# Kernel optimization log

Hardware: AMD Instinct MI355X
Metric: run time of the kernel (lower is better)

The kernel has to match this reference:

```python
import jax, jax.numpy as jnp
import numpy as np

D = 2048          # hidden_size
I = 8192          # expert_intermediate_size
E = 8             # num_experts
TOP_K = 2
N_CONST = 2       # ConstantExpert count (CONSTANT=2); experts: [copy, zero, ce0, ce1, shared_mlp x (E-4)]


def setup_inputs() -> dict:
    key = jax.random.key(0)
    ks = jax.random.split(key, 9)
    s = 0.02
    return {
        "hidden_states": jax.random.normal(ks[0], (2, 2048, D), dtype=jnp.float32),
        "gate_w1": jax.random.normal(ks[1], (D, E * 8), dtype=jnp.float32) * s,
        "gate_w2": jax.random.normal(ks[2], (E * 8, E), dtype=jnp.float32) * s,
        "ce_wg": jax.random.normal(ks[3], (N_CONST, D, 2), dtype=jnp.float32) * s,
        "ce_const": jax.random.normal(ks[4], (N_CONST, D), dtype=jnp.float32),
        "w_gate": jax.random.normal(ks[5], (D, I), dtype=jnp.float32) * s,
        "w_up": jax.random.normal(ks[6], (D, I), dtype=jnp.float32) * s,
        "w_down": jax.random.normal(ks[7], (I, D), dtype=jnp.float32) * s,
    }


def reference(hidden_states, gate_w1, gate_w2, ce_wg, ce_const, w_gate, w_up, w_down):
    B, S, d = hidden_states.shape
    x = hidden_states.reshape(-1, d).astype(jnp.float32)          # [N, D] tokens

    # Router: MLP gate (fp32) -> softmax -> top-2
    router_logits = jnp.tanh(x @ gate_w1) @ gate_w2               # [N, E]
    probs = jax.nn.softmax(router_logits, axis=-1)
    topw, topi = jax.lax.top_k(probs, TOP_K)                      # [N, 2]
    # mask out last expert (idx == E-1), renormalize
    topw = jnp.where(topi == E - 1, jnp.zeros_like(topw), topw)
    topw = topw / jnp.sum(topw, axis=-1, keepdims=True)
    # per-expert combined routing weight (top-k indices are distinct)
    pe = jnp.sum(topw[..., None] * jax.nn.one_hot(topi, E, dtype=topw.dtype), axis=1)  # [N, E]

    def const_expert(wg, c):
        cw = jax.nn.softmax(x @ wg, axis=-1)                      # [N, 2]
        return cw[:, :1] * x + cw[:, 1:] * c[None, :]

    # shared SwiGLU expert (all dense experts share the same weights in the source)
    swiglu = (jax.nn.silu(x @ w_gate) * (x @ w_up)) @ w_down      # [N, D]

    out = (pe[:, 0:1] * x                                          # CopyExpert (expert 1 = ZeroExpert contributes 0)
           + pe[:, 2:3] * const_expert(ce_wg[0], ce_const[0])
           + pe[:, 3:4] * const_expert(ce_wg[1], ce_const[1])
           + jnp.sum(pe[:, 4:], axis=1, keepdims=True) * swiglu)   # shared dense experts 4..E-1
    return out.reshape(B, S, d), router_logits
```

## Files before the change

kernel.cpp:

```cpp
#include <hip/hip_runtime.h>
#include <stdint.h>
#include <stddef.h>

#define TOKS 4096
#define DH   2048
#define DI   8192

typedef __attribute__((ext_vector_type(8))) short short8v;
typedef __attribute__((ext_vector_type(4))) short short4v;
typedef __attribute__((ext_vector_type(4))) float floatx4;

__device__ __forceinline__ float b2f(short s) {
  union { unsigned u; float f; } v;
  v.u = ((unsigned)(unsigned short)s) << 16;
  return v.f;
}
__device__ __forceinline__ short f2b(float f) {
  union { float f; unsigned u; } v; v.f = f;
  unsigned r = (v.u + 0x7fffu + ((v.u >> 16) & 1u)) >> 16;
  return (short)(unsigned short)r;
}
__device__ __forceinline__ void gload_lds16(const void* g, void* l) {
  __builtin_amdgcn_global_load_lds((const __attribute__((address_space(1))) void*)g,
                                   (__attribute__((address_space(3))) void*)l, 16, 0, 0);
}

__global__ __launch_bounds__(256) void cvt_f32_to_bf16(const float* __restrict__ in,
                                                       short* __restrict__ out) {
  size_t i = (size_t)blockIdx.x * 256 + threadIdx.x;
  floatx4 v = *(const floatx4*)&in[i * 4];
  short4v o;
  o[0] = f2b(v[0]); o[1] = f2b(v[1]); o[2] = f2b(v[2]); o[3] = f2b(v[3]);
  *(short4v*)&out[i * 4] = o;
}

__global__ __launch_bounds__(256) void transpose_to_bf16(const float* __restrict__ in,
                                                         short* __restrict__ out,
                                                         int K, int N,
                                                         int rstride, int roff) {
  __shared__ float tile[32][33];
  const int n0 = blockIdx.x * 32, k0 = blockIdx.y * 32;
  const int tx = threadIdx.x & 31, ty = threadIdx.x >> 5;
#pragma unroll
  for (int yy = 0; yy < 32; yy += 8)
    tile[ty + yy][tx] = in[(size_t)(k0 + ty + yy) * N + n0 + tx];
  __syncthreads();
#pragma unroll
  for (int yy = 0; yy < 32; yy += 8)
    out[((size_t)(n0 + ty + yy) * rstride + roff) * K + k0 + tx] = f2b(tile[tx][ty + yy]);
}

#define RT_TPB 8
__global__ __launch_bounds__(256) void router_kernel(const float* __restrict__ x,
                                                     const float* __restrict__ gw1,
                                                     const float* __restrict__ gw2,
                                                     const float* __restrict__ cwg,
                                                     float* __restrict__ logits_out,
                                                     float* __restrict__ coef) {
  const int wave = threadIdx.x >> 6, lane = threadIdx.x & 63;
  const int tok0 = blockIdx.x * RT_TPB;
  __shared__ float xs[RT_TPB][512];
  __shared__ float ll[RT_TPB][8];
  __shared__ float cd[RT_TPB][4];

  float tj[2] = {0.f, 0.f};
  float cda[2][4] = {{0.f,0.f,0.f,0.f},{0.f,0.f,0.f,0.f}};

  const int st = threadIdx.x >> 5;
  const int sl = threadIdx.x & 31;

  for (int c = 0; c < 4; ++c) {
    const int dbase = c * 512;
#pragma unroll
    for (int r = 0; r < 4; ++r) {
      const int idx = r * 128 + sl * 4;
      *(floatx4*)&xs[st][idx] = *(const floatx4*)&x[(size_t)(tok0 + st) * DH + dbase + idx];
    }
    __syncthreads();
    for (int d = 0; d < 512; ++d) {
      const float g = gw1[(size_t)(dbase + d) * 64 + lane];
      tj[0] += xs[wave * 2 + 0][d] * g;
      tj[1] += xs[wave * 2 + 1][d] * g;
    }
#pragma unroll
    for (int dq = 0; dq < 8; ++dq) {
      const int d = dq * 64 + lane;
      const float w0 = cwg[(size_t)(dbase + d) * 2 + 0];
      const float w1 = cwg[(size_t)(dbase + d) * 2 + 1];
      const float w2 = cwg[(size_t)DH * 2 + (dbase + d) * 2 + 0];
      const float w3 = cwg[(size_t)DH * 2 + (dbase + d) * 2 + 1];
#pragma unroll
      for (int t = 0; t < 2; ++t) {
        const float xv = xs[wave * 2 + t][d];
        cda[t][0] += xv * w0; cda[t][1] += xv * w1;
        cda[t][2] += xv * w2; cda[t][3] += xv * w3;
      }
    }
    __syncthreads();
  }

#pragma unroll
  for (int t = 0; t < 2; ++t) {
    const float th = tanhf(tj[t]);
#pragma unroll
    for (int e = 0; e < 8; ++e) {
      float p = th * gw2[lane * 8 + e];
      for (int off = 32; off; off >>= 1) p += __shfl_xor(p, off);
      if (lane == 0) ll[wave * 2 + t][e] = p;
    }
#pragma unroll
    for (int dd = 0; dd < 4; ++dd) {
      float p = cda[t][dd];
      for (int off = 32; off; off >>= 1) p += __shfl_xor(p, off);
      if (lane == 0) cd[wave * 2 + t][dd] = p;
    }
  }
  __syncthreads();

  if (threadIdx.x < RT_TPB) {
    const int t = threadIdx.x;
    const int gtok = tok0 + t;
    float l[8];
#pragma unroll
    for (int e = 0; e < 8; ++e) l[e] = ll[t][e];
#pragma unroll
    for (int e = 0; e < 8; ++e) logits_out[(size_t)gtok * 8 + e] = l[e];
    float m = l[0];
#pragma unroll
    for (int e = 1; e < 8; ++e) m = fmaxf(m, l[e]);
    float p[8], s = 0.f;
#pragma unroll
    for (int e = 0; e < 8; ++e) { p[e] = expf(l[e] - m); s += p[e]; }
#pragma unroll
    for (int e = 0; e < 8; ++e) p[e] /= s;
    int i1 = 0;
#pragma unroll
    for (int e = 1; e < 8; ++e) if (p[e] > p[i1]) i1 = e;
    int i2 = -1;
#pragma unroll
    for (int e = 0; e < 8; ++e) {
      if (e == i1) continue;
      if (i2 < 0 || p[e] > p[i2]) i2 = e;
    }
    float w1 = (i1 == 7) ? 0.f : p[i1];
    float w2 = (i2 == 7) ? 0.f : p[i2];
    const float nrm = w1 + w2;
    w1 /= nrm; w2 /= nrm;
    float pe[8];
#pragma unroll
    for (int e = 0; e < 8; ++e) pe[e] = 0.f;
    pe[i1] += w1; pe[i2] += w2;
    const float cw00 = 1.f / (1.f + expf(cd[t][1] - cd[t][0]));
    const float cw10 = 1.f / (1.f + expf(cd[t][3] - cd[t][2]));
    coef[gtok * 4 + 0] = pe[0] + pe[2] * cw00 + pe[3] * cw10;
    coef[gtok * 4 + 1] = pe[2] * (1.f - cw00);
    coef[gtok * 4 + 2] = pe[3] * (1.f - cw10);
    coef[gtok * 4 + 3] = pe[4] + pe[5] + pe[6] + pe[7];
  }
}

__global__ __launch_bounds__(512, 2) void gemm1_gu_silu(const short* __restrict__ A,
                                                        const short* __restrict__ Bt,
                                                        short* __restrict__ H,
                                                        int K, int lda, int ldb) {
  __shared__ __align__(16) short As[2][256 * 64];
  __shared__ __align__(16) short Bs[2][256 * 64];

  const int wave = threadIdx.x >> 6;
  const int lane = threadIdx.x & 63;
  const int wm64 = (wave >> 2) * 64;
  const int wn32 = (wave & 3) * 32;
  const int l15 = lane & 15;
  const int quad = lane >> 4;
  const int rq = l15 & 7;
  const int qoff0 = (quad ^ rq) * 8;
  const int qoff1 = ((4 + quad) ^ rq) * 8;

  const int srow = lane >> 3;
  const int scol = ((lane & 7) ^ srow) * 8;

  const int cpx = gridDim.x >> 3;
  const int wg = ((int)blockIdx.x & 7) * cpx + ((int)blockIdx.x >> 3);
  const int m0 = (wg & 15) * 256;
  const int n0 = (wg >> 4) * 256;

  const short* pA = A + (size_t)(m0 + wave * 16 + srow) * lda + scol;
  const short* pB = Bt + (size_t)(n0 + wave * 16 + srow) * ldb + scol;

  floatx4 acc[8][4];
#pragma unroll
  for (int i = 0; i < 8; ++i)
#pragma unroll
    for (int j = 0; j < 4; ++j) acc[i][j] = (floatx4)0.f;

  short8v a[4][2];
  short8v b[4][2];

#define STAGE_A(buf, half, k0)                                                  \
  {                                                                             \
    _Pragma("unroll") for (int g = 0; g < 2; ++g)                               \
        gload_lds16(pA + (size_t)((half) * 128 + g * 8) * lda + (k0),           \
                    &As[buf][((half) * 128 + wave * 16 + g * 8) * 64]);         \
  }
#define STAGE_B(buf, half, k0)                                                  \
  {                                                                             \
    _Pragma("unroll") for (int g = 0; g < 2; ++g)                               \
        gload_lds16(pB + (size_t)((half) * 128 + g * 8) * ldb + (k0),           \
                    &Bs[buf][((half) * 128 + wave * 16 + g * 8) * 64]);         \
  }
#define READ_A(buf, half)                                                       \
  {                                                                             \
    _Pragma("unroll") for (int mi = 0; mi < 4; ++mi) {                          \
      const int r = (half) * 128 + wm64 + mi * 16 + l15;                        \
      a[mi][0] = *(const short8v*)&As[buf][r * 64 + qoff0];                     \
      a[mi][1] = *(const short8v*)&As[buf][r * 64 + qoff1];                     \
    }                                                                           \
  }
#define READ_BALL(buf)                                                          \
  {                                                                             \
    _Pragma("unroll") for (int h = 0; h < 2; ++h)                               \
    _Pragma("unroll") for (int ni = 0; ni < 2; ++ni) {                          \
      const int r = h * 128 + wn32 + ni * 16 + l15;                             \
      b[h * 2 + ni][0] = *(const short8v*)&Bs[buf][r * 64 + qoff0];             \
      b[h * 2 + ni][1] = *(const short8v*)&Bs[buf][r * 64 + qoff1];             \
    }                                                                           \
  }
#define MFMA_H(mh)                                                              \
  {                                                                             \
    __builtin_amdgcn_s_setprio(1);                                              \
    _Pragma("unroll") for (int kk = 0; kk < 2; ++kk)                            \
    _Pragma("unroll") for (int mi = 0; mi < 4; ++mi)                            \
    _Pragma("unroll") for (int ni = 0; ni < 4; ++ni)                            \
        acc[(mh) * 4 + mi][ni] = __builtin_amdgcn_mfma_f32_16x16x32_bf16(       \
            a[mi][kk], b[ni][kk], acc[(mh) * 4 + mi][ni], 0, 0, 0);             \
    __builtin_amdgcn_s_setprio(0);                                              \
  }
#define BAR __builtin_amdgcn_s_barrier()
#define LGKM0 asm volatile("s_waitcnt lgkmcnt(0)" ::: "memory")
#define VMC(n) asm volatile("s_waitcnt vmcnt(" #n ")" ::: "memory")

#define KTILE(t, MODE)                                                          \
  {                                                                             \
    const int buf = (t) & 1, nbuf = buf ^ 1;                                    \
    const int k1 = ((t) + 1) * 64, k2 = ((t) + 2) * 64;                         \
    (void)k1; (void)k2; (void)nbuf;                                             \
                                                          \
    READ_A(buf, 0); READ_BALL(buf);                                             \
    if (MODE <= 1) { STAGE_B(nbuf, 1, k1); STAGE_A(nbuf, 1, k1); }              \
    BAR; LGKM0; MFMA_H(0); BAR;                                                 \
                                                          \
    READ_A(buf, 1);                                                             \
    if (MODE == 0) { STAGE_A(buf, 0, k2); STAGE_B(buf, 0, k2); VMC(4); }        \
    if (MODE == 1) { VMC(0); }                                                  \
    BAR; LGKM0; MFMA_H(1); BAR;                                                 \
  }

  STAGE_A(0, 0, 0); STAGE_B(0, 0, 0); STAGE_B(0, 1, 0); STAGE_A(0, 1, 0);
  STAGE_A(1, 0, 64); STAGE_B(1, 0, 64);
  VMC(4);
  BAR;

  const int NT = K >> 6;
  for (int t = 0; t < NT - 2; ++t) KTILE(t, 0);
  KTILE(NT - 2, 1);
  KTILE(NT - 1, 2);

#undef KTILE
#undef STAGE_A
#undef STAGE_B
#undef READ_A
#undef READ_BALL
#undef MFMA_H

  const int q4 = quad * 4;
#pragma unroll
  for (int mi = 0; mi < 8; ++mi) {
    const int row0 = m0 + (mi >> 2) * 128 + wm64 + (mi & 3) * 16 + q4;
#pragma unroll
    for (int ni = 0; ni < 4; ++ni) {
      const int col = n0 + (ni >> 1) * 128 + wn32 + (ni & 1) * 16 + l15;
#pragma unroll
      for (int rg = 0; rg < 4; ++rg) {
        const float v = acc[mi][ni][rg];
        const float p = __shfl_xor(v, 1);
        if ((l15 & 1) == 0) {
          const float hv = (v / (1.f + __expf(-v))) * p;
          H[(size_t)(row0 + rg) * DI + (col >> 1)] = f2b(hv);
        }
      }
    }
  }
}

__device__ __forceinline__ void gemm_mainloop(const short* __restrict__ A,
                                              const short* __restrict__ Bt,
                                              int K, int lda, int ldb,
                                              int m0, int n0,
                                              short* As, short* Bs,
                                              floatx4 (&acc)[4][4]) {
  const int wave = threadIdx.x >> 6;
  const int lane = threadIdx.x & 63;
  const int srow = lane >> 3;
  const int scol = ((lane & 7) ^ srow) * 8;
  const int wm = (wave & 1) * 64;
  const int wn = (wave >> 1) * 64;
  const int l15 = lane & 15;
  const int quad = lane >> 4;
  const int q0 = ((quad ^ (l15 & 7)) * 8);

  for (int k0 = 0; k0 < K; k0 += 64) {
#pragma unroll
    for (int q = 0; q < 4; ++q) {
      const int chunk = wave * 4 + q;
      const int row = chunk * 8 + srow;
      gload_lds16(A + (size_t)(m0 + row) * lda + k0 + scol, &As[chunk * 8 * 64]);
      gload_lds16(Bt + (size_t)(n0 + row) * ldb + k0 + scol, &Bs[chunk * 8 * 64]);
    }
    __syncthreads();
#pragma unroll
    for (int kk = 0; kk < 2; ++kk) {
      const int qo = q0 ^ (kk * 32);
      short8v af[4], bf[4];
#pragma unroll
      for (int i = 0; i < 4; ++i) {
        af[i] = *(const short8v*)&As[(wm + i * 16 + l15) * 64 + qo];
        bf[i] = *(const short8v*)&Bs[(wn + i * 16 + l15) * 64 + qo];
      }
#pragma unroll
      for (int mi = 0; mi < 4; ++mi)
#pragma unroll
        for (int ni = 0; ni < 4; ++ni)
          acc[mi][ni] = __builtin_amdgcn_mfma_f32_16x16x32_bf16(af[mi], bf[ni],
                                                                acc[mi][ni], 0, 0, 0);
    }
    __syncthreads();
  }
}

__global__ __launch_bounds__(256) void gemm_bt_moe(const short* __restrict__ A,
                                                   const short* __restrict__ Bt,
                                                   float* __restrict__ out,
                                                   const float* __restrict__ x,
                                                   const float* __restrict__ cc,
                                                   const float* __restrict__ coef,
                                                   int K, int lda, int ldb) {
  __shared__ short As[128 * 64];
  __shared__ short Bs[128 * 64];
  floatx4 acc[4][4];
#pragma unroll
  for (int a = 0; a < 4; ++a)
#pragma unroll
    for (int b = 0; b < 4; ++b) acc[a][b] = (floatx4)0.0f;
  const int lin = blockIdx.y * gridDim.x + blockIdx.x;
  const int m0 = (lin & 31) * 128, n0 = (lin >> 5) * 128;
  gemm_mainloop(A, Bt, K, lda, ldb, m0, n0, As, Bs, acc);
  const int wave = threadIdx.x >> 6, lane = threadIdx.x & 63;
  const int wm = (wave & 1) * 64, wn = (wave >> 1) * 64;
  const int l15 = lane & 15, q4 = (lane >> 4) * 4;
#pragma unroll
  for (int mi = 0; mi < 4; ++mi) {
    const int row0 = m0 + wm + mi * 16 + q4;
#pragma unroll
    for (int ni = 0; ni < 4; ++ni) {
      const int col = n0 + wn + ni * 16 + l15;
      const float c0v = cc[col];
      const float c1v = cc[DH + col];
#pragma unroll
      for (int rg = 0; rg < 4; ++rg) {
        const int row = row0 + rg;
        const floatx4 cf = *(const floatx4*)&coef[row * 4];
        out[(size_t)row * DH + col] =
            cf[0] * x[(size_t)row * DH + col] + cf[1] * c0v + cf[2] * c1v +
            cf[3] * acc[mi][ni][rg];
      }
    }
  }
}

extern "C" void kernel_launch(void* const* d_in, const int* in_sizes, int n_in,
                              void* d_out, int out_size, void* d_ws, size_t ws_size,
                              hipStream_t stream) {
  const float* x   = (const float*)d_in[0];
  const float* gw1 = (const float*)d_in[1];
  const float* gw2 = (const float*)d_in[2];
  const float* cwg = (const float*)d_in[3];
  const float* cc  = (const float*)d_in[4];
  const float* wg  = (const float*)d_in[5];
  const float* wu  = (const float*)d_in[6];
  const float* wd  = (const float*)d_in[7];
  float* out = (float*)d_out;
  float* logits_out = out + (size_t)TOKS * DH;

  char* ws = (char*)d_ws;
  short* xb    = (short*)(ws);
  short* wgwuT = (short*)(ws + 16777216);
  short* wdT   = (short*)(ws + 16777216 + 67108864);
  short* H     = (short*)(ws + 117440512);
  float* coef  = (float*)(ws + 117440512 + 67108864);

  cvt_f32_to_bf16<<<(TOKS * DH) / (256 * 4), 256, 0, stream>>>(x, xb);
  transpose_to_bf16<<<dim3(DI / 32, DH / 32), 256, 0, stream>>>(wg, wgwuT, DH, DI, 2, 0);
  transpose_to_bf16<<<dim3(DI / 32, DH / 32), 256, 0, stream>>>(wu, wgwuT, DH, DI, 2, 1);
  transpose_to_bf16<<<dim3(DH / 32, DI / 32), 256, 0, stream>>>(wd, wdT, DI, DH, 1, 0);
  router_kernel<<<TOKS / RT_TPB, 256, 0, stream>>>(x, gw1, gw2, cwg, logits_out, coef);
  gemm1_gu_silu<<<dim3((TOKS / 256) * ((2 * DI) / 256)), 512, 0, stream>>>(
      xb, wgwuT, H, DH, DH, DH);
  gemm_bt_moe<<<dim3(DH / 128, TOKS / 128), 256, 0, stream>>>(
      H, wdT, out, x, cc, coef, DI, DI, DI);
}
```

Measured before the change: 806.9 us.

## Drop per-half barriers and explicit lgkm waits; interleave LDS fragment reads in GEMM

Each K-tile of the gate/up GEMM now has two workgroup barriers instead of four. The explicit lgkmcnt(0) waits are removed, so the compiler can insert fine-grained waits per operand. LDS fragment reads are split and reordered so the A and B fragments needed by the first MFMAs arrive first, letting matrix work start before all reads finish. Compiler-only memory fences around the barrier keep ordering. The risk is an LDS race between waves reading one half of a buffer and the asynchronous stage that overwrites it, if the remaining barriers do not cover every hazard.

```diff
diff --git a/kernel.cpp b/kernel.cpp
--- a/kernel.cpp
+++ b/kernel.cpp
@@ -208,23 +208,10 @@
         gload_lds16(pB + (size_t)((half) * 128 + g * 8) * ldb + (k0),           \
                     &Bs[buf][((half) * 128 + wave * 16 + g * 8) * 64]);         \
   }
-#define READ_A(buf, half)                                                       \
-  {                                                                             \
-    _Pragma("unroll") for (int mi = 0; mi < 4; ++mi) {                          \
-      const int r = (half) * 128 + wm64 + mi * 16 + l15;                        \
-      a[mi][0] = *(const short8v*)&As[buf][r * 64 + qoff0];                     \
-      a[mi][1] = *(const short8v*)&As[buf][r * 64 + qoff1];                     \
-    }                                                                           \
-  }
-#define READ_BALL(buf)                                                          \
-  {                                                                             \
-    _Pragma("unroll") for (int h = 0; h < 2; ++h)                               \
-    _Pragma("unroll") for (int ni = 0; ni < 2; ++ni) {                          \
-      const int r = h * 128 + wn32 + ni * 16 + l15;                             \
-      b[h * 2 + ni][0] = *(const short8v*)&Bs[buf][r * 64 + qoff0];             \
-      b[h * 2 + ni][1] = *(const short8v*)&Bs[buf][r * 64 + qoff1];             \
-    }                                                                           \
-  }
+#define RD_A(mi, half, kk)                                                      \
+  a[mi][kk] = *(const short8v*)&As[buf][((half) * 128 + wm64 + (mi) * 16 + l15) * 64 + ((kk) ? qoff1 : qoff0)]
+#define RD_B(j, kk)                                                             \
+  b[j][kk] = *(const short8v*)&Bs[buf][(((j) >> 1) * 128 + wn32 + ((j) & 1) * 16 + l15) * 64 + ((kk) ? qoff1 : qoff0)]
 #define MFMA_H(mh)                                                              \
   {                                                                             \
     __builtin_amdgcn_s_setprio(1);                                              \
@@ -235,8 +222,8 @@
             a[mi][kk], b[ni][kk], acc[(mh) * 4 + mi][ni], 0, 0, 0);             \
     __builtin_amdgcn_s_setprio(0);                                              \
   }
-#define BAR __builtin_amdgcn_s_barrier()
-#define LGKM0 asm volatile("s_waitcnt lgkmcnt(0)" ::: "memory")
+#define FENCE asm volatile("" ::: "memory")
+#define BAR do { FENCE; __builtin_amdgcn_s_barrier(); FENCE; } while (0)
 #define VMC(n) asm volatile("s_waitcnt vmcnt(" #n ")" ::: "memory")
 
 #define KTILE(t, MODE)                                                          \
@@ -244,15 +231,21 @@
     const int buf = (t) & 1, nbuf = buf ^ 1;                                    \
     const int k1 = ((t) + 1) * 64, k2 = ((t) + 2) * 64;                         \
     (void)k1; (void)k2; (void)nbuf;                                             \
-                                                          \
-    READ_A(buf, 0); READ_BALL(buf);                                             \
+       \
+    RD_A(0, 0, 0); RD_B(0, 0); RD_B(1, 0); RD_B(2, 0); RD_B(3, 0);              \
+    RD_A(1, 0, 0); RD_A(2, 0, 0); RD_A(3, 0, 0);                                \
+    RD_A(0, 0, 1); RD_B(0, 1); RD_B(1, 1); RD_B(2, 1); RD_B(3, 1);              \
+    RD_A(1, 0, 1); RD_A(2, 0, 1); RD_A(3, 0, 1);                                \
     if (MODE <= 1) { STAGE_B(nbuf, 1, k1); STAGE_A(nbuf, 1, k1); }              \
-    BAR; LGKM0; MFMA_H(0); BAR;                                                 \
-                                                          \
-    READ_A(buf, 1);                                                             \
+    MFMA_H(0);                                                                  \
+    BAR;                                                                        \
+                          \
+    RD_A(0, 1, 0); RD_A(1, 1, 0); RD_A(2, 1, 0); RD_A(3, 1, 0);                 \
+    RD_A(0, 1, 1); RD_A(1, 1, 1); RD_A(2, 1, 1); RD_A(3, 1, 1);                 \
     if (MODE == 0) { STAGE_A(buf, 0, k2); STAGE_B(buf, 0, k2); VMC(4); }        \
     if (MODE == 1) { VMC(0); }                                                  \
-    BAR; LGKM0; MFMA_H(1); BAR;                                                 \
+    MFMA_H(1);                                                                  \
+    BAR;                                                                        \
   }
 
   STAGE_A(0, 0, 0); STAGE_B(0, 0, 0); STAGE_B(0, 1, 0); STAGE_A(0, 1, 0);
@@ -268,8 +261,8 @@
 #undef KTILE
 #undef STAGE_A
 #undef STAGE_B
-#undef READ_A
-#undef READ_BALL
+#undef RD_A
+#undef RD_B
 #undef MFMA_H
 
   const int q4 = quad * 4;
```

Result: no change. 791.1 us (-2.0%).
